# Optimization experiments

Measured on AMD Instinct MI355X. Metric: run time of the kernel, lower is better.

## Reference

```python
import jax, jax.numpy as jnp
import numpy as np

NUM_NODES = 100000
NUM_EDGES = 640000
D_IN = 128
D_OUT = 128


def setup_inputs() -> dict:
    key = jax.random.key(0)
    k_x, k_s, k_t, k_w, k_lin = jax.random.split(key, 5)
    x = jax.random.normal(k_x, (NUM_NODES, D_IN), dtype=jnp.float32)
    source = jax.random.randint(k_s, (NUM_EDGES,), 0, NUM_NODES, dtype=jnp.int32)
    target = jax.random.randint(k_t, (NUM_EDGES,), 0, NUM_NODES, dtype=jnp.int32)
    edge_weights = jax.random.uniform(k_w, (NUM_EDGES,), dtype=jnp.float32)
    # nn.Linear weight, shape (out, in), kaiming-uniform-ish init
    bound = 1.0 / np.sqrt(D_IN)
    W = jax.random.uniform(k_lin, (D_OUT, D_IN), dtype=jnp.float32, minval=-bound, maxval=bound)
    return {"x": x, "W": W, "edge_weights": edge_weights, "source": source, "target": target}


def reference(x, W, edge_weights, source, target):
    # LinearMessageCreator: project all nodes first (as in the torch code), then gather per edge
    h = jnp.einsum("nd,od->no", x, W)            # (num_nodes, d_out)
    msg = h[source] * edge_weights[:, None]       # (num_edges, d_out)
    # SumAggregator: scatter-add messages into target nodes
    delta = jax.ops.segment_sum(msg, target, num_segments=x.shape[0])
    # OnlyUpdate: return aggregated messages
    return delta
```

## Files before the change

kernel.cpp:

```cpp
#include <hip/hip_runtime.h>
#include <hip/hip_bf16.h>

#define NN 100000
#define NE 640000
#define D 128

#define SCAN_CHUNK 1024
#define NBLK ((NN + SCAN_CHUNK - 1) / SCAN_CHUNK)

#define OFF_COUNTS  0u
#define OFF_OFFSETS 400000u
#define OFF_CURSOR  800016u
#define OFF_BSUM    1200016u
#define OFF_BSUMEX  1200528u
#define OFF_PE      1201040u
#define WS_T2       6321040u
#define OFF_XB      6321040u
#define WS_FULL     31921040u

typedef __attribute__((ext_vector_type(8))) short bf16x8;
typedef __attribute__((ext_vector_type(4))) float f32x4;

__device__ __forceinline__ float bflo(unsigned u) { return __uint_as_float(u << 16); }
__device__ __forceinline__ float bfhi(unsigned u) { return __uint_as_float(u & 0xffff0000u); }
__device__ __forceinline__ unsigned bfpk(float x, float y) {
    __hip_bfloat16 bx = __float2bfloat16(x), by = __float2bfloat16(y);
    return (unsigned)(*(unsigned short*)&bx) | ((unsigned)(*(unsigned short*)&by) << 16);
}

__global__ __launch_bounds__(256) void k_hist(const int* __restrict__ tgt,
                                              int* __restrict__ counts) {
    int e = blockIdx.x * 256 + threadIdx.x;
    if (e < NE) atomicAdd(&counts[tgt[e]], 1);
}

__global__ __launch_bounds__(256) void k_scan_part(const int* __restrict__ counts,
                                                   int* __restrict__ bsum) {
    __shared__ int sd[256];
    int b = blockIdx.x, t = threadIdx.x;
    int base = b * SCAN_CHUNK + t * 4;
    int s = 0;
    #pragma unroll
    for (int k = 0; k < 4; ++k) { int i = base + k; s += (i < NN) ? counts[i] : 0; }
    sd[t] = s; __syncthreads();
    for (int off = 128; off > 0; off >>= 1) {
        if (t < off) sd[t] += sd[t + off];
        __syncthreads();
    }
    if (t == 0) bsum[b] = sd[0];
}

__global__ __launch_bounds__(128) void k_scan_mid(const int* __restrict__ bsum,
                                                  int* __restrict__ bsumex,
                                                  int* __restrict__ offsets) {
    __shared__ int sd[128];
    int t = threadIdx.x;
    int v = (t < NBLK) ? bsum[t] : 0;
    sd[t] = v; __syncthreads();
    for (int off = 1; off < 128; off <<= 1) {
        int tmp = (t >= off) ? sd[t - off] : 0;
        __syncthreads();
        sd[t] += tmp;
        __syncthreads();
    }
    if (t < NBLK) bsumex[t] = sd[t] - v;
    if (t == 0) offsets[NN] = NE;
}

__global__ __launch_bounds__(256) void k_scan_final(const int* __restrict__ counts,
                                                    const int* __restrict__ bsumex,
                                                    int* __restrict__ offsets,
                                                    int* __restrict__ cursor) {
    __shared__ int sd[256];
    int b = blockIdx.x, t = threadIdx.x;
    int base = b * SCAN_CHUNK + t * 4;
    int c[4]; int s = 0;
    #pragma unroll
    for (int k = 0; k < 4; ++k) { int i = base + k; c[k] = (i < NN) ? counts[i] : 0; s += c[k]; }
    sd[t] = s; __syncthreads();
    for (int off = 1; off < 256; off <<= 1) {
        int tmp = (t >= off) ? sd[t - off] : 0;
        __syncthreads();
        sd[t] += tmp;
        __syncthreads();
    }
    int run = sd[t] - s + bsumex[b];
    #pragma unroll
    for (int k = 0; k < 4; ++k) {
        int i = base + k;
        if (i < NN) { offsets[i] = run; cursor[i] = run; }
        run += c[k];
    }
}

__global__ __launch_bounds__(256) void k_fill(const int* __restrict__ src,
                                              const int* __restrict__ tgt,
                                              const float* __restrict__ ew,
                                              int* __restrict__ cursor,
                                              int2* __restrict__ pe) {
    int e = blockIdx.x * 256 + threadIdx.x;
    if (e < NE) {
        int t = tgt[e];
        int p = atomicAdd(&cursor[t], 1);
        pe[p] = make_int2(src[e], __float_as_int(ew[e]));
    }
}

__global__ __launch_bounds__(256) void k_conv(const float* __restrict__ x,
                                              unsigned* __restrict__ xb) {
    int i = blockIdx.x * 256 + threadIdx.x;
    if (i < NN * 64) {
        float2 v = ((const float2*)x)[i];
        xb[i] = bfpk(v.x, v.y);
    }
}

__global__ __launch_bounds__(256) void k_gather_bf(const unsigned* __restrict__ xb,
                                                   const int* __restrict__ offsets,
                                                   const int2* __restrict__ pe,
                                                   float* __restrict__ out) {
    int wid = blockIdx.x * 4 + (threadIdx.x >> 6);
    int lane = threadIdx.x & 63;
    if (wid >= NN) return;
    int beg = offsets[wid], end = offsets[wid + 1];
    float a0 = 0.f, a1 = 0.f;
    int2 e = (beg < end) ? pe[beg] : make_int2(0, 0);
    for (int i = beg; i < end; ++i) {
        int2 en = (i + 1 < end) ? pe[i + 1] : make_int2(0, 0);
        unsigned v = xb[(size_t)e.x * 64 + lane];
        float w = __int_as_float(e.y);
        a0 = fmaf(bflo(v), w, a0);
        a1 = fmaf(bfhi(v), w, a1);
        e = en;
    }
    ((float2*)out)[(size_t)wid * 64 + lane] = make_float2(a0, a1);
}

__global__ __launch_bounds__(256) void k_gather_f32(const float* __restrict__ x,
                                                    const int* __restrict__ offsets,
                                                    const int2* __restrict__ pe,
                                                    float* __restrict__ out) {
    int wid = blockIdx.x * 4 + (threadIdx.x >> 6);
    int lane = threadIdx.x & 63;
    if (wid >= NN) return;
    int beg = offsets[wid], end = offsets[wid + 1];
    const float2* x2 = (const float2*)x;
    float a0 = 0.f, a1 = 0.f;
    int2 e = (beg < end) ? pe[beg] : make_int2(0, 0);
    for (int i = beg; i < end; ++i) {
        int2 en = (i + 1 < end) ? pe[i + 1] : make_int2(0, 0);
        float2 v = x2[(size_t)e.x * 64 + lane];
        float w = __int_as_float(e.y);
        a0 = fmaf(v.x, w, a0);
        a1 = fmaf(v.y, w, a1);
        e = en;
    }
    ((float2*)out)[(size_t)wid * 64 + lane] = make_float2(a0, a1);
}

#define KP 136

__global__ __launch_bounds__(256) void k_project_mfma(const float* __restrict__ W,
                                                      float* __restrict__ io) {
    __shared__ unsigned short Wb[D][KP];
    __shared__ unsigned short As[64][KP];

    const int tid = threadIdx.x;
    const long nb = (long)blockIdx.x * 64;

    const float4* W4 = (const float4*)W;
    #pragma unroll
    for (int it = 0; it < 16; ++it) {
        int idx = it * 256 + tid;
        int f = idx >> 5, kq = idx & 31;
        float4 v = W4[idx];
        *(uint2*)&Wb[f][kq * 4] = make_uint2(bfpk(v.x, v.y), bfpk(v.z, v.w));
    }
    const float4* io4 = (const float4*)io;
    #pragma unroll
    for (int it = 0; it < 8; ++it) {
        int idx = it * 256 + tid;
        int n = idx >> 5, kq = idx & 31;
        long node = nb + n;
        float4 v = (node < NN) ? io4[node * 32 + kq]
                               : make_float4(0.f, 0.f, 0.f, 0.f);
        *(uint2*)&As[n][kq * 4] = make_uint2(bfpk(v.x, v.y), bfpk(v.z, v.w));
    }
    __syncthreads();

    const int w  = tid >> 6;
    const int l  = tid & 63;
    const int lr = l & 15;
    const int lg = l >> 4;
    const int r0 = w * 16;

    bf16x8 afrag[4];
    #pragma unroll
    for (int ks = 0; ks < 4; ++ks)
        afrag[ks] = *(const bf16x8*)&As[r0 + lr][ks * 32 + lg * 8];

    #pragma unroll
    for (int ct = 0; ct < 8; ++ct) {
        f32x4 acc = {0.f, 0.f, 0.f, 0.f};
        #pragma unroll
        for (int ks = 0; ks < 4; ++ks) {
            bf16x8 bfrag = *(const bf16x8*)&Wb[ct * 16 + lr][ks * 32 + lg * 8];
            acc = __builtin_amdgcn_mfma_f32_16x16x32_bf16(afrag[ks], bfrag, acc, 0, 0, 0);
        }
        #pragma unroll
        for (int r = 0; r < 4; ++r) {
            long gn = nb + r0 + lg * 4 + r;
            if (gn < NN) io[gn * D + ct * 16 + lr] = acc[r];
        }
    }
}

__global__ __launch_bounds__(256) void gcn_scatter(const float* __restrict__ x,
                                                   const float* __restrict__ ew,
                                                   const int* __restrict__ src,
                                                   const int* __restrict__ tgt,
                                                   float* __restrict__ out) {
    int tid = blockIdx.x * 256 + threadIdx.x;
    int e = tid >> 5;
    int t = tid & 31;
    if (e >= NE) return;
    int s = src[e];
    int g = tgt[e];
    float w = ew[e];
    float4 xv = reinterpret_cast<const float4*>(x)[s * 32 + t];
    float* dst = out + (size_t)g * D + (t << 2);
    atomicAdd(dst + 0, xv.x * w);
    atomicAdd(dst + 1, xv.y * w);
    atomicAdd(dst + 2, xv.z * w);
    atomicAdd(dst + 3, xv.w * w);
}

extern "C" void kernel_launch(void* const* d_in, const int* in_sizes, int n_in,
                              void* d_out, int out_size, void* d_ws, size_t ws_size,
                              hipStream_t stream) {
    const float* x   = (const float*)d_in[0];
    const float* W   = (const float*)d_in[1];
    const float* ew  = (const float*)d_in[2];
    const int*   src = (const int*)d_in[3];
    const int*   tgt = (const int*)d_in[4];
    float* out = (float*)d_out;

    if (ws_size >= WS_T2) {
        char* ws = (char*)d_ws;
        int*  counts  = (int*)(ws + OFF_COUNTS);
        int*  offsets = (int*)(ws + OFF_OFFSETS);
        int*  cursor  = (int*)(ws + OFF_CURSOR);
        int*  bsum    = (int*)(ws + OFF_BSUM);
        int*  bsumex  = (int*)(ws + OFF_BSUMEX);
        int2* pe      = (int2*)(ws + OFF_PE);

        hipMemsetAsync(counts, 0, (size_t)NN * sizeof(int), stream);
        k_hist<<<(NE + 255) / 256, 256, 0, stream>>>(tgt, counts);
        k_scan_part<<<NBLK, 256, 0, stream>>>(counts, bsum);
        k_scan_mid<<<1, 128, 0, stream>>>(bsum, bsumex, offsets);
        k_scan_final<<<NBLK, 256, 0, stream>>>(counts, bsumex, offsets, cursor);
        k_fill<<<(NE + 255) / 256, 256, 0, stream>>>(src, tgt, ew, cursor, pe);

        if (ws_size >= WS_FULL) {
            unsigned* xb = (unsigned*)(ws + OFF_XB);
            k_conv<<<(NN * 64 + 255) / 256, 256, 0, stream>>>(x, xb);
            k_gather_bf<<<(NN + 3) / 4, 256, 0, stream>>>(xb, offsets, pe, out);
        } else {
            k_gather_f32<<<(NN + 3) / 4, 256, 0, stream>>>(x, offsets, pe, out);
        }
    } else {
        hipMemsetAsync(out, 0, (size_t)out_size * sizeof(float), stream);
        gcn_scatter<<<(NE * 32 + 255) / 256, 256, 0, stream>>>(x, ew, src, tgt, out);
    }

    k_project_mfma<<<(NN + 63) / 64, 256, 0, stream>>>(W, out);
}
```

Baseline: 261.1 us.

## Fuse CSR gather with MFMA projection and merge fill/convert kernels

Merges the edge-fill and fp32-to-bf16 conversion into a single launch by splitting the grid into block ranges. Fuses the per-node gather with the bf16 MFMA projection: each 512-thread block gathers 64 nodes into shared memory, then multiplies them by W there. This removes the fp32 intermediate write and re-read of the aggregated features, and drops two launches. In exchange, each warp now handles 8 nodes serially, which may lower memory-level parallelism in the gather, and the larger blocks may lower occupancy.

```diff
diff --git a/kernel.cpp b/kernel.cpp
--- a/kernel.cpp
+++ b/kernel.cpp
@@ -90,6 +90,33 @@
         int i = base + k;
         if (i < NN) { offsets[i] = run; cursor[i] = run; }
         run += c[k];
+    }
+}
+
+#define FILL_BLKS ((NE + 255) / 256)
+#define CONV_BLKS ((NN * 64 + 255) / 256)
+
+__global__ __launch_bounds__(256) void k_fill_conv(const int* __restrict__ src,
+                                                   const int* __restrict__ tgt,
+                                                   const float* __restrict__ ew,
+                                                   int* __restrict__ cursor,
+                                                   int2* __restrict__ pe,
+                                                   const float* __restrict__ x,
+                                                   unsigned* __restrict__ xb) {
+    int b = blockIdx.x;
+    if (b < FILL_BLKS) {
+        int e = b * 256 + threadIdx.x;
+        if (e < NE) {
+            int t = tgt[e];
+            int p = atomicAdd(&cursor[t], 1);
+            pe[p] = make_int2(src[e], __float_as_int(ew[e]));
+        }
+    } else {
+        int i = (b - FILL_BLKS) * 256 + threadIdx.x;
+        if (i < NN * 64) {
+            float2 v = ((const float2*)x)[i];
+            xb[i] = bfpk(v.x, v.y);
+        }
     }
 }
 
@@ -106,34 +133,75 @@
     }
 }
 
-__global__ __launch_bounds__(256) void k_conv(const float* __restrict__ x,
-                                              unsigned* __restrict__ xb) {
-    int i = blockIdx.x * 256 + threadIdx.x;
-    if (i < NN * 64) {
-        float2 v = ((const float2*)x)[i];
-        xb[i] = bfpk(v.x, v.y);
-    }
-}
-
-__global__ __launch_bounds__(256) void k_gather_bf(const unsigned* __restrict__ xb,
-                                                   const int* __restrict__ offsets,
-                                                   const int2* __restrict__ pe,
-                                                   float* __restrict__ out) {
-    int wid = blockIdx.x * 4 + (threadIdx.x >> 6);
-    int lane = threadIdx.x & 63;
-    if (wid >= NN) return;
-    int beg = offsets[wid], end = offsets[wid + 1];
-    float a0 = 0.f, a1 = 0.f;
-    int2 e = (beg < end) ? pe[beg] : make_int2(0, 0);
-    for (int i = beg; i < end; ++i) {
-        int2 en = (i + 1 < end) ? pe[i + 1] : make_int2(0, 0);
-        unsigned v = xb[(size_t)e.x * 64 + lane];
-        float w = __int_as_float(e.y);
-        a0 = fmaf(bflo(v), w, a0);
-        a1 = fmaf(bfhi(v), w, a1);
-        e = en;
-    }
-    ((float2*)out)[(size_t)wid * 64 + lane] = make_float2(a0, a1);
+#define KP 136
+
+__global__ __launch_bounds__(512) void k_gather_project(const unsigned* __restrict__ xb,
+                                                        const int* __restrict__ offsets,
+                                                        const int2* __restrict__ pe,
+                                                        const float* __restrict__ W,
+                                                        float* __restrict__ out) {
+    __shared__ __align__(16) unsigned short Wb[D][KP];
+    __shared__ __align__(16) unsigned short As[64][KP];
+
+    const int tid = threadIdx.x;
+    const long nb = (long)blockIdx.x * 64;
+
+    const float4* W4 = (const float4*)W;
+    #pragma unroll
+    for (int it = 0; it < 8; ++it) {
+        int idx = it * 512 + tid;
+        int f = idx >> 5, kq = idx & 31;
+        float4 v = W4[idx];
+        *(uint2*)&Wb[f][kq * 4] = make_uint2(bfpk(v.x, v.y), bfpk(v.z, v.w));
+    }
+
+    const int w = tid >> 6;
+    const int lane = tid & 63;
+
+    for (int j = 0; j < 8; ++j) {
+        int n = w * 8 + j;
+        long node = nb + n;
+        int beg = 0, end = 0;
+        if (node < NN) { beg = offsets[node]; end = offsets[node + 1]; }
+        float a0 = 0.f, a1 = 0.f;
+        int2 e = (beg < end) ? pe[beg] : make_int2(0, 0);
+        for (int i = beg; i < end; ++i) {
+            int2 en = (i + 1 < end) ? pe[i + 1] : make_int2(0, 0);
+            unsigned v = xb[(size_t)e.x * 64 + lane];
+            float wt = __int_as_float(e.y);
+            a0 = fmaf(bflo(v), wt, a0);
+            a1 = fmaf(bfhi(v), wt, a1);
+            e = en;
+        }
+        *(unsigned*)&As[n][lane * 2] = bfpk(a0, a1);
+    }
+    __syncthreads();
+
+    const int lr = lane & 15;
+    const int lg = lane >> 4;
+    const int r0 = (w >> 1) * 16;
+    const int ct0 = (w & 1) * 4;
+
+    bf16x8 afrag[4];
+    #pragma unroll
+    for (int ks = 0; ks < 4; ++ks)
+        afrag[ks] = *(const bf16x8*)&As[r0 + lr][ks * 32 + lg * 8];
+
+    #pragma unroll
+    for (int c = 0; c < 4; ++c) {
+        int ct = ct0 + c;
+        f32x4 acc = {0.f, 0.f, 0.f, 0.f};
+        #pragma unroll
+        for (int ks = 0; ks < 4; ++ks) {
+            bf16x8 bfrag = *(const bf16x8*)&Wb[ct * 16 + lr][ks * 32 + lg * 8];
+            acc = __builtin_amdgcn_mfma_f32_16x16x32_bf16(afrag[ks], bfrag, acc, 0, 0, 0);
+        }
+        #pragma unroll
+        for (int r = 0; r < 4; ++r) {
+            long gn = nb + r0 + lg * 4 + r;
+            if (gn < NN) out[gn * D + ct * 16 + lr] = acc[r];
+        }
+    }
 }
 
 __global__ __launch_bounds__(256) void k_gather_f32(const float* __restrict__ x,
@@ -158,12 +226,10 @@
     ((float2*)out)[(size_t)wid * 64 + lane] = make_float2(a0, a1);
 }
 
-#define KP 136
-
 __global__ __launch_bounds__(256) void k_project_mfma(const float* __restrict__ W,
                                                       float* __restrict__ io) {
-    __shared__ unsigned short Wb[D][KP];
-    __shared__ unsigned short As[64][KP];
+    __shared__ __align__(16) unsigned short Wb[D][KP];
+    __shared__ __align__(16) unsigned short As[64][KP];
 
     const int tid = threadIdx.x;
     const long nb = (long)blockIdx.x * 64;
@@ -259,19 +325,19 @@
         k_scan_part<<<NBLK, 256, 0, stream>>>(counts, bsum);
         k_scan_mid<<<1, 128, 0, stream>>>(bsum, bsumex, offsets);
         k_scan_final<<<NBLK, 256, 0, stream>>>(counts, bsumex, offsets, cursor);
-        k_fill<<<(NE + 255) / 256, 256, 0, stream>>>(src, tgt, ew, cursor, pe);
 
         if (ws_size >= WS_FULL) {
             unsigned* xb = (unsigned*)(ws + OFF_XB);
-            k_conv<<<(NN * 64 + 255) / 256, 256, 0, stream>>>(x, xb);
-            k_gather_bf<<<(NN + 3) / 4, 256, 0, stream>>>(xb, offsets, pe, out);
+            k_fill_conv<<<FILL_BLKS + CONV_BLKS, 256, 0, stream>>>(src, tgt, ew, cursor, pe, x, xb);
+            k_gather_project<<<(NN + 63) / 64, 512, 0, stream>>>(xb, offsets, pe, W, out);
         } else {
+            k_fill<<<FILL_BLKS, 256, 0, stream>>>(src, tgt, ew, cursor, pe);
             k_gather_f32<<<(NN + 3) / 4, 256, 0, stream>>>(x, offsets, pe, out);
+            k_project_mfma<<<(NN + 63) / 64, 256, 0, stream>>>(W, out);
         }
     } else {
         hipMemsetAsync(out, 0, (size_t)out_size * sizeof(float), stream);
         gcn_scatter<<<(NE * 32 + 255) / 256, 256, 0, stream>>>(x, ew, src, tgt, out);
-    }
-
-    k_project_mfma<<<(NN + 63) / 64, 256, 0, stream>>>(W, out);
-}
+        k_project_mfma<<<(NN + 63) / 64, 256, 0, stream>>>(W, out);
+    }
+}
```

After: 264.8 us. Within noise of the previous version (+1.4%).
